# Optimization experiments

Measured on AMD Instinct MI355X. Metric: run time of the kernel, lower is better.

The kernel has to match this reference:

```python
import jax, jax.numpy as jnp
import numpy as np
import math

D_MODEL = 2048
N_HEADS = 16
D_FF = 8192
SEQ = 2048
BATCH = 2
THETA = 10000.0
EPS = 1e-5


def _rope(x, pos):
    # x: [B, H, S, d_k] ; pos: [B, S] int
    d = x.shape[-1]
    inv_freq = 1.0 / (THETA ** (jnp.arange(0, d, 2, dtype=jnp.float32) / d))  # [d/2]
    ang = pos[..., None].astype(jnp.float32) * inv_freq  # [B, S, d/2]
    cos = jnp.cos(ang)[:, None, :, :, None]  # [B,1,S,d/2,1]
    sin = jnp.sin(ang)[:, None, :, :, None]
    xr = x.reshape(*x.shape[:-1], d // 2, 2)
    x1, x2 = xr[..., 0], xr[..., 1]
    rot = jnp.stack((-x2, x1), axis=-1)  # rotate pairs
    out = xr * cos + rot * sin
    return out.reshape(x.shape)


def _trunc_normal(key, shape, in_f, out_f):
    std = math.sqrt(2.0 / (in_f + out_f))
    return jax.random.truncated_normal(key, -3.0, 3.0, shape, jnp.float32) * std


def setup_inputs() -> dict:
    key = jax.random.key(0)
    ks = jax.random.split(key, 8)
    x = jax.random.normal(ks[0], (BATCH, SEQ, D_MODEL), jnp.float32)
    token_positions = jnp.sort(jax.random.randint(ks[1], (BATCH, SEQ), 0, SEQ), axis=-1)
    W_qkv = _trunc_normal(ks[2], (3 * D_MODEL, D_MODEL), D_MODEL, 3 * D_MODEL)
    W_o = _trunc_normal(ks[3], (D_MODEL, D_MODEL), D_MODEL, D_MODEL)
    W1 = _trunc_normal(ks[4], (D_FF, D_MODEL), D_MODEL, D_FF)
    W3 = _trunc_normal(ks[5], (D_FF, D_MODEL), D_MODEL, D_FF)
    W2 = _trunc_normal(ks[6], (D_MODEL, D_FF), D_FF, D_MODEL)
    g1 = jnp.ones((D_MODEL,), jnp.float32)
    g2 = jnp.ones((D_MODEL,), jnp.float32)
    return {"x": x, "token_positions": token_positions, "W_qkv": W_qkv, "W_o": W_o,
            "g1": g1, "g2": g2, "W1": W1, "W3": W3, "W2": W2}


def _rmsnorm(x, g):
    xf = x.astype(jnp.float32)
    rms = jnp.sqrt(jnp.mean(xf * xf, axis=-1, keepdims=True) + EPS)
    return (xf / rms * g).astype(x.dtype)


def reference(x, token_positions, W_qkv, W_o, g1, g2, W1, W3, W2):
    B, S, D = x.shape
    H = N_HEADS
    dk = D // H
    # --- attention sublayer ---
    h = _rmsnorm(x, g1)
    qkv = jnp.einsum('bsi,oi->bso', h, W_qkv)  # [B,S,3D]
    q, k, v = jnp.split(qkv, 3, axis=-1)
    to_heads = lambda t: t.reshape(B, S, H, dk).transpose(0, 2, 1, 3)  # [B,H,S,dk]
    q, k, v = to_heads(q), to_heads(k), to_heads(v)
    q = _rope(q, token_positions)
    k = _rope(k, token_positions)
    scores = jnp.einsum('bhnd,bhmd->bhnm', q, k) / math.sqrt(dk)  # [B,H,S,S]
    mask = jnp.tril(jnp.ones((S, S), dtype=bool))
    scores = jnp.where(mask, scores, -jnp.inf)
    attn = jax.nn.softmax(scores, axis=-1)
    o = jnp.einsum('bhnm,bhmd->bhnd', attn, v)
    o = o.transpose(0, 2, 1, 3).reshape(B, S, D)
    x = x + jnp.einsum('bsi,oi->bso', o, W_o)
    # --- SwiGLU FFN sublayer ---
    h2 = _rmsnorm(x, g2)
    x1 = jnp.einsum('bsi,oi->bso', h2, W1)
    x3 = jnp.einsum('bsi,oi->bso', h2, W3)
    x = x + jnp.einsum('bsi,oi->bso', jax.nn.silu(x1) * x3, W2)
    return x
```

## Files before the change

### kernel.cpp

```cpp
#include <hip/hip_runtime.h>

#define DEV __device__ __forceinline__

typedef __bf16 bf16x8 __attribute__((ext_vector_type(8)));
typedef float f32x4 __attribute__((ext_vector_type(4)));
typedef unsigned short u16x8 __attribute__((ext_vector_type(8)));

DEV unsigned short f2bf(float f) {
  unsigned int u = __float_as_uint(f);
  u += 0x7fffu + ((u >> 16) & 1u);
  return (unsigned short)(u >> 16);
}
DEV float bf2f(unsigned short h) {
  return __uint_as_float(((unsigned int)h) << 16);
}
DEV void gload16(const void* g, void* l) {
  __builtin_amdgcn_global_load_lds(
      (const __attribute__((address_space(1))) unsigned int*)g,
      (__attribute__((address_space(3))) unsigned int*)l, 16, 0, 0);
}
DEV f32x4 mfma16(bf16x8 a, bf16x8 b, f32x4 c) {
  return __builtin_amdgcn_mfma_f32_16x16x32_bf16(a, b, c, 0, 0, 0);
}

#define SB   __builtin_amdgcn_s_barrier()
#define SCH  __builtin_amdgcn_sched_barrier(0)
#define LGKM0 asm volatile("s_waitcnt lgkmcnt(0)" ::: "memory")
#define LGKM4 asm volatile("s_waitcnt lgkmcnt(4)" ::: "memory")
#define VM6  asm volatile("s_waitcnt vmcnt(6)" ::: "memory")
#define PRIO1 __builtin_amdgcn_s_setprio(1)
#define PRIO0 __builtin_amdgcn_s_setprio(0)

__global__ __launch_bounds__(256) void k_cvt(const float* __restrict__ in,
                                             unsigned short* __restrict__ out, int n8) {
  const int stride = gridDim.x * 256;
  for (int i = blockIdx.x * 256 + threadIdx.x; i < n8; i += stride) {
    const float4* p = (const float4*)(in + (long)i * 8);
    const float4 a = p[0], b = p[1];
    u16x8 o = { f2bf(a.x), f2bf(a.y), f2bf(a.z), f2bf(a.w),
                f2bf(b.x), f2bf(b.y), f2bf(b.z), f2bf(b.w) };
    *(u16x8*)(out + (long)i * 8) = o;
  }
}

__global__ __launch_bounds__(256) void k_rmsnorm(const float* __restrict__ x,
                                                 const float* __restrict__ g,
                                                 unsigned short* __restrict__ out) {
  const int row = blockIdx.x;
  const int t = threadIdx.x;
  const float4* xr = (const float4*)(x + (long)row * 2048);
  const float4 a = xr[t * 2], c = xr[t * 2 + 1];
  float ss = a.x * a.x + a.y * a.y + a.z * a.z + a.w * a.w +
             c.x * c.x + c.y * c.y + c.z * c.z + c.w * c.w;
#pragma unroll
  for (int o = 32; o > 0; o >>= 1) ss += __shfl_down(ss, o);
  __shared__ float ws4[4];
  __shared__ float invs;
  if ((t & 63) == 0) ws4[t >> 6] = ss;
  __syncthreads();
  if (t == 0) invs = 1.0f / sqrtf((ws4[0] + ws4[1] + ws4[2] + ws4[3]) * (1.0f / 2048.0f) + 1e-5f);
  __syncthreads();
  const float inv = invs;
  const float4* gr = (const float4*)g;
  const float4 g0 = gr[t * 2], g1v = gr[t * 2 + 1];
  u16x8 o8 = { f2bf(a.x * inv * g0.x),  f2bf(a.y * inv * g0.y),
               f2bf(a.z * inv * g0.z),  f2bf(a.w * inv * g0.w),
               f2bf(c.x * inv * g1v.x), f2bf(c.y * inv * g1v.y),
               f2bf(c.z * inv * g1v.z), f2bf(c.w * inv * g1v.w) };
  *(u16x8*)(out + (long)row * 2048 + t * 8) = o8;
}

__global__ __launch_bounds__(256) void k_rmsnorm2(const float* __restrict__ xa,
                                                  const float* __restrict__ xb,
                                                  const float* __restrict__ g,
                                                  float* __restrict__ xsum,
                                                  unsigned short* __restrict__ out) {
  const int row = blockIdx.x;
  const int t = threadIdx.x;
  const float4* ar = (const float4*)(xa + (long)row * 2048);
  const float4* br = (const float4*)(xb + (long)row * 2048);
  float4 a = ar[t * 2], c = ar[t * 2 + 1];
  const float4 pa = br[t * 2], pc = br[t * 2 + 1];
  a.x += pa.x; a.y += pa.y; a.z += pa.z; a.w += pa.w;
  c.x += pc.x; c.y += pc.y; c.z += pc.z; c.w += pc.w;
  float4* sr = (float4*)(xsum + (long)row * 2048);
  sr[t * 2] = a; sr[t * 2 + 1] = c;
  float ss = a.x * a.x + a.y * a.y + a.z * a.z + a.w * a.w +
             c.x * c.x + c.y * c.y + c.z * c.z + c.w * c.w;
#pragma unroll
  for (int o = 32; o > 0; o >>= 1) ss += __shfl_down(ss, o);
  __shared__ float ws4[4];
  __shared__ float invs;
  if ((t & 63) == 0) ws4[t >> 6] = ss;
  __syncthreads();
  if (t == 0) invs = 1.0f / sqrtf((ws4[0] + ws4[1] + ws4[2] + ws4[3]) * (1.0f / 2048.0f) + 1e-5f);
  __syncthreads();
  const float inv = invs;
  const float4* gr = (const float4*)g;
  const float4 g0 = gr[t * 2], g1v = gr[t * 2 + 1];
  u16x8 o8 = { f2bf(a.x * inv * g0.x),  f2bf(a.y * inv * g0.y),
               f2bf(a.z * inv * g0.z),  f2bf(a.w * inv * g0.w),
               f2bf(c.x * inv * g1v.x), f2bf(c.y * inv * g1v.y),
               f2bf(c.z * inv * g1v.z), f2bf(c.w * inv * g1v.w) };
  *(u16x8*)(out + (long)row * 2048 + t * 8) = o8;
}

template <int EPI>
__global__ __launch_bounds__(512, 2) void k_gemm256(
    const unsigned short* __restrict__ A, const unsigned short* __restrict__ B,
    unsigned short* __restrict__ outBF, float* __restrict__ outF,
    const float* __restrict__ resid, const unsigned short* __restrict__ aux,
    float* __restrict__ partial, const int* __restrict__ tp,
    unsigned short* __restrict__ p2, unsigned short* __restrict__ p3,
    int M, int N, int K, int Keff) {
  __shared__ __align__(16) unsigned short lds[2][2][2][128][64];
  const int tid = threadIdx.x;
  const int wid = tid >> 6, lane = tid & 63;
  const int wr = wid >> 2, wc = wid & 3;
  const int fr = lane & 15, g4 = lane >> 4;

  const int nwg = gridDim.x;
  int bid = blockIdx.x;
  { int q = nwg >> 3, r = nwg & 7, xcd = bid & 7, lo = bid >> 3;
    bid = (xcd < r ? xcd * (q + 1) : r * (q + 1) + (xcd - r) * q) + lo; }
  int tile = bid, ks = 0;
  if constexpr (EPI == 3) { ks = bid & 1; tile = bid >> 1; }
  const int nxb = N >> 8;
  const int bx = tile % nxb, by = tile / nxb;
  const int arow0 = by << 8, bcol0 = bx << 8;
  const int NT = Keff >> 6;

  const int srow = tid >> 3;
  const int sg = (tid & 7) ^ (srow & 7);
  const unsigned short* Asrc = A + (long)(arow0 + srow) * K + (long)ks * Keff + (sg << 3);
  const unsigned short* Bsrc = B + (long)(bcol0 + srow) * K + (long)ks * Keff + (sg << 3);

  const int posk0 = (g4 ^ (lane & 7)) << 3;
  const int posk1 = ((4 + g4) ^ (lane & 7)) << 3;

  f32x4 acc[8][4] = {};
  bf16x8 a[4][2], b0[2][2], b1[2][2];

#define STAGE(SRC, xs, bufi, mat, h)                                            \
  { const unsigned short* s_ = (SRC) + (long)(h) * 128 * K + (long)(xs) * 64;   \
    unsigned short* d_ = &lds[bufi][mat][h][0][0] + wid * 512;                  \
    gload16(s_, d_);                                                            \
    gload16(s_ + (long)64 * K, d_ + 4096); }
#define RD_A(BA, mh)                                                            \
  _Pragma("unroll") for (int m_ = 0; m_ < 4; ++m_) {                            \
    const unsigned short* p_ = (BA) + ((mh) * 64 + m_ * 16 + fr) * 64;          \
    a[m_][0] = *(const bf16x8*)(p_ + posk0);                                    \
    a[m_][1] = *(const bf16x8*)(p_ + posk1); }
#define RD_B(BB, arr, nh)                                                       \
  _Pragma("unroll") for (int n_ = 0; n_ < 2; ++n_) {                            \
    const unsigned short* p_ = (BB) + ((nh) * 32 + n_ * 16 + fr) * 64;          \
    arr[n_][0] = *(const bf16x8*)(p_ + posk0);                                  \
    arr[n_][1] = *(const bf16x8*)(p_ + posk1); }
#define MM(mh, nh, Bv)                                                          \
  _Pragma("unroll") for (int k_ = 0; k_ < 2; ++k_)                              \
  _Pragma("unroll") for (int m_ = 0; m_ < 4; ++m_)                              \
  _Pragma("unroll") for (int n_ = 0; n_ < 2; ++n_)                              \
    acc[(mh)*4+m_][(nh)*2+n_] = mfma16(a[m_][k_], Bv[n_][k_], acc[(mh)*4+m_][(nh)*2+n_]);

  STAGE(Asrc, 0, 0, 0, 0);
  STAGE(Asrc, 0, 0, 0, 1);
  STAGE(Bsrc, 0, 0, 1, 0);
  STAGE(Bsrc, 0, 0, 1, 1);
  { const int x1p = (NT > 1) ? 1 : 0;
    STAGE(Bsrc, x1p, 1, 1, 0);
    STAGE(Bsrc, x1p, 1, 1, 1);
    STAGE(Asrc, x1p, 1, 0, 0); }
  VM6; SCH; SB; SCH;
  {
    const unsigned short* baseA = &lds[0][0][wr][0][0];
    const unsigned short* baseB = &lds[0][1][wc >> 1][0][0] + (wc & 1) * 4096;
    RD_A(baseA, 0); RD_B(baseB, b0, 0);
  }

  for (int t = 0; t < NT; ++t) {
    const unsigned short* baseA = &lds[t & 1][0][wr][0][0];
    const unsigned short* baseB = &lds[t & 1][1][wc >> 1][0][0] + (wc & 1) * 4096;
    const unsigned short* baseA2 = &lds[(t + 1) & 1][0][wr][0][0];
    const unsigned short* baseB2 = &lds[(t + 1) & 1][1][wc >> 1][0][0] + (wc & 1) * 4096;
    const int x1 = (t + 1 < NT) ? t + 1 : NT - 1;
    const int x2i = (t + 2 < NT) ? t + 2 : NT - 1;
    const int bn = (t + 1) & 1, bc = t & 1;

    SB;
    RD_B(baseB, b1, 1);
    STAGE(Asrc, x1, bn, 0, 1);
    LGKM4; SCH;
    PRIO1; MM(0, 0, b0); PRIO0;
    LGKM0; SCH;
    PRIO1; MM(0, 1, b1); PRIO0;

    SB;
    RD_A(baseA, 1);
    STAGE(Bsrc, x2i, bc, 1, 0);
    LGKM0; SCH;
    PRIO1; MM(1, 1, b1); PRIO0;

    SB;
    STAGE(Asrc, x2i, bc, 0, 0);
    STAGE(Bsrc, x2i, bc, 1, 1);
    PRIO1; MM(1, 0, b0); PRIO0;
    VM6; SCH; SB; SCH;
    RD_A(baseA2, 0);
    RD_B(baseB2, b0, 0);
  }
#undef STAGE
#undef RD_A
#undef RD_B
#undef MM

  const int er = g4 << 2;
  if constexpr (EPI == 4) {
    const int region = bcol0 >> 11;
#pragma unroll
    for (int m = 0; m < 8; ++m) {
      const int grow = arow0 + wr * 128 + m * 16 + er;
      float pos4[4];
#pragma unroll
      for (int r = 0; r < 4; ++r)
        pos4[r] = (region < 2) ? (float)tp[grow + r] : 0.f;
#pragma unroll
      for (int n = 0; n < 4; ++n) {
        const int gcol = bcol0 + wc * 64 + n * 16 + fr;
        const int d = gcol & 127;
        const float invf = __expf((float)(d >> 1) * -0.14391156831212787f);
        const int h = (gcol >> 7) & 15;
#pragma unroll
        for (int r = 0; r < 4; ++r) {
          const int row = grow + r;
          const int b = row >> 11, s = row & 2047;
          float v = acc[m][n][r];
          if (region < 2) {
            const float other = __shfl_xor(v, 1);
            float cc, sn;
            __sincosf(pos4[r] * invf, &sn, &cc);
            v = (d & 1) ? (v * cc + other * sn) : (v * cc - other * sn);
          }
          unsigned short* dst = (region == 0) ? outBF : (region == 1 ? p2 : p3);
          dst[((long)((b << 4) + h) * 2048 + s) * 128 + d] = f2bf(v);
        }
      }
    }
  } else {
#pragma unroll
    for (int m = 0; m < 8; ++m) {
#pragma unroll
      for (int n = 0; n < 4; ++n) {
        const int grow = arow0 + wr * 128 + m * 16 + er;
        const int gcol = bcol0 + wc * 64 + n * 16 + fr;
#pragma unroll
        for (int r = 0; r < 4; ++r) {
          const long idx = (long)(grow + r) * N + gcol;
          const float v = acc[m][n][r];
          if constexpr (EPI == 0) {
            outBF[idx] = f2bf(v);
          } else if constexpr (EPI == 1) {
            outF[idx] = resid[idx] + v;
          } else if constexpr (EPI == 2) {
            const float x1v = bf2f(aux[idx]);
            const float sl = x1v / (1.0f + __expf(-x1v));
            outBF[idx] = f2bf(sl * v);
          } else {
            if (ks == 0) outF[idx] = resid[idx] + v;
            else         partial[idx] = v;
          }
        }
      }
    }
  }
}

__global__ __launch_bounds__(512, 1) void k_gemm_n128(
    const unsigned short* __restrict__ A, const unsigned short* __restrict__ B,
    float* __restrict__ outF, const float* __restrict__ resid, int M, int N, int K) {
  __shared__ __align__(16) unsigned short lds[3][384 * 64];
  const int tid = threadIdx.x;
  const int wid = tid >> 6, lane = tid & 63;
  const int wr = wid >> 1, wc = wid & 1;
  const int fr = lane & 15, g4 = lane >> 4;

  const int nwg = gridDim.x;
  int bid = blockIdx.x;
  { int q = nwg >> 3, r = nwg & 7, xcd = bid & 7, lo = bid >> 3;
    bid = (xcd < r ? xcd * (q + 1) : r * (q + 1) + (xcd - r) * q) + lo; }
  const int nxb = N >> 7;
  const int bx = bid % nxb, by = bid / nxb;
  const int arow0 = by << 8, bcol0 = bx << 7;
  const int NT = K >> 6;

  const int srow = tid >> 3;
  const int sg = (tid & 7) ^ (srow & 7);
  const unsigned short* Asrc = A + (long)(arow0 + srow) * K + (sg << 3);
  const unsigned short* Bsrc = B + (long)(bcol0 + srow) * K + (sg << 3);

  const int posk0 = (g4 ^ (lane & 7)) << 3;
  const int posk1 = ((4 + g4) ^ (lane & 7)) << 3;

  f32x4 acc[4][4] = {};
  bf16x8 a[4][2], bl[2][2], bh[2][2];

#define SITE_A(xs, bufi, s)                                                    \
  gload16(Asrc + (long)((s) * 64) * K + (long)(xs) * 64,                       \
          &lds[bufi][(s) * 4096] + wid * 512);
#define SITE_B(xs, bufi, s)                                                    \
  gload16(Bsrc + (long)((s) * 64) * K + (long)(xs) * 64,                       \
          &lds[bufi][16384 + (s) * 4096] + wid * 512);
#define RDA(BUF)                                                               \
  _Pragma("unroll") for (int m_ = 0; m_ < 4; ++m_) {                           \
    const unsigned short* p_ = (BUF) + (wr * 64 + m_ * 16 + fr) * 64;          \
    a[m_][0] = *(const bf16x8*)(p_ + posk0);                                   \
    a[m_][1] = *(const bf16x8*)(p_ + posk1); }
#define RDB(BUF, arr, off)                                                     \
  _Pragma("unroll") for (int n_ = 0; n_ < 2; ++n_) {                           \
    const unsigned short* p_ = (BUF) + 16384 + (wc * 64 + (off) + n_ * 16 + fr) * 64; \
    arr[n_][0] = *(const bf16x8*)(p_ + posk0);                                 \
    arr[n_][1] = *(const bf16x8*)(p_ + posk1); }
#define MMN(nh, Bv)                                                            \
  _Pragma("unroll") for (int k_ = 0; k_ < 2; ++k_)                             \
  _Pragma("unroll") for (int m_ = 0; m_ < 4; ++m_)                             \
  _Pragma("unroll") for (int n_ = 0; n_ < 2; ++n_)                             \
    acc[m_][(nh)*2+n_] = mfma16(a[m_][k_], Bv[n_][k_], acc[m_][(nh)*2+n_]);

  SITE_A(0, 0, 0); SITE_A(0, 0, 1); SITE_A(0, 0, 2); SITE_A(0, 0, 3);
  SITE_B(0, 0, 0); SITE_B(0, 0, 1);
  { const int x1p = (NT > 1) ? 1 : 0;
    SITE_A(x1p, 1, 0); SITE_A(x1p, 1, 1); SITE_A(x1p, 1, 2); SITE_A(x1p, 1, 3);
    SITE_B(x1p, 1, 0); SITE_B(x1p, 1, 1); }
  VM6; SCH; SB; SCH;
  RDA(lds[0]); RDB(lds[0], bl, 0);

  for (int t = 0; t < NT; ++t) {
    const unsigned short* bufb = lds[t % 3];
    const unsigned short* bufn = lds[(t + 1) % 3];
    const int bn = (t + 2) % 3;
    const int xs = (t + 2 < NT) ? t + 2 : NT - 1;

    SB;
    RDB(bufb, bh, 32);
    SITE_A(xs, bn, 0); SITE_A(xs, bn, 1);
    LGKM4; SCH;
    PRIO1; MMN(0, bl); PRIO0;
    SITE_A(xs, bn, 2); SITE_A(xs, bn, 3); SITE_B(xs, bn, 0); SITE_B(xs, bn, 1);
    LGKM0; SCH;
    PRIO1; MMN(1, bh); PRIO0;
    VM6; SCH; SB; SCH;
    RDA(bufn); RDB(bufn, bl, 0);
  }
#undef SITE_A
#undef SITE_B
#undef RDA
#undef RDB
#undef MMN

  const int er = g4 << 2;
#pragma unroll
  for (int m = 0; m < 4; ++m) {
#pragma unroll
    for (int n = 0; n < 4; ++n) {
      const int grow = arow0 + wr * 64 + m * 16 + er;
      const int gcol = bcol0 + wc * 64 + n * 16 + fr;
#pragma unroll
      for (int r = 0; r < 4; ++r) {
        const long idx = (long)(grow + r) * N + gcol;
        outF[idx] = resid[idx] + acc[m][n][r];
      }
    }
  }
}

__global__ __launch_bounds__(256) void k_vtrans(const unsigned short* __restrict__ Vh,
                                                unsigned short* __restrict__ Vt, int S) {
  __shared__ __align__(16) unsigned short t[128 * 72];
  const int bh = blockIdx.x;
  const int s0 = blockIdx.y << 6;
  const int tid = threadIdx.x;
  const int sl = tid >> 2, c4 = tid & 3;
#pragma unroll
  for (int it = 0; it < 4; ++it) {
    const int chunk = c4 * 4 + it;
    u16x8 v = *(const u16x8*)(Vh + ((long)bh * S + s0 + sl) * 128 + chunk * 8);
#pragma unroll
    for (int jj = 0; jj < 8; ++jj) t[(chunk * 8 + jj) * 72 + sl] = v[jj];
  }
  __syncthreads();
  const int d = tid >> 1, half = tid & 1;
  unsigned short* dst = Vt + ((long)bh * 128 + d) * S + s0 + half * 32;
  const unsigned short* srcr = &t[d * 72 + half * 32];
#pragma unroll
  for (int u = 0; u < 4; ++u)
    *(u16x8*)(dst + u * 8) = *(const u16x8*)(srcr + u * 8);
}

__global__ __launch_bounds__(256) void k_attn(const unsigned short* __restrict__ Q,
                                              const unsigned short* __restrict__ Kh,
                                              const unsigned short* __restrict__ Vt,
                                              unsigned short* __restrict__ O, int S) {
  __shared__ __align__(16) unsigned short lds_k[64 * 128];
  __shared__ __align__(16) unsigned short lds_v[128 * 64];
  __shared__ __align__(16) unsigned short lds_p[4 * 16 * 64];
  const int bh = blockIdx.x;
  const int b = bh >> 4, h = bh & 15;
  const int qt = gridDim.y - 1 - blockIdx.y;
  const int q0 = qt << 6;
  const int tid = threadIdx.x, w = tid >> 6, lane = tid & 63;
  const int fr = lane & 15, g4 = lane >> 4;

  bf16x8 qf[4];
  {
    const unsigned short* qb = Q + ((long)bh * S + q0 + w * 16 + fr) * 128 + (g4 << 3);
#pragma unroll
    for (int kk = 0; kk < 4; ++kk) qf[kk] = *(const bf16x8*)(qb + kk * 32);
  }

  f32x4 accO[8] = {};
  float mrow[4], lrow[4];
#pragma unroll
  for (int r = 0; r < 4; ++r) { mrow[r] = -1e30f; lrow[r] = 0.f; }

  const int k_row = (w << 4) + g4;
  const int k_cb = fr << 4;
  const int v_row = (w << 5) + (lane >> 3);
  const int v_cb = (lane & 7) << 4;
  const long kbase = (long)bh * S * 128;
  const long vbase = (long)bh * 128 * S;

  const int ntile = qt + 1;
  for (int it = 0; it < ntile; ++it) {
    const int kv0 = it << 6;
#pragma unroll
    for (int j = 0; j < 4; ++j) {
      const int kr = k_row + j * 4;
      const int kc = k_cb ^ ((kr & 7) << 4);
      gload16(Kh + kbase + (long)(kv0 + kr) * 128 + (kc >> 1), &lds_k[w * 2048 + j * 512]);
      const int vr = v_row + j * 8;
      const int vc = v_cb ^ ((vr & 7) << 4);
      gload16(Vt + vbase + (long)vr * S + kv0 + (vc >> 1), &lds_v[w * 2048 + j * 512]);
    }
    __syncthreads();

    f32x4 sc[4] = {};
#pragma unroll
    for (int kk = 0; kk < 4; ++kk) {
      const int kb = (kk << 6) + (g4 << 4);
#pragma unroll
      for (int n = 0; n < 4; ++n) {
        const int krw = n * 16 + fr;
        const int swz = (krw & 7) << 4;
        bf16x8 kf = *(const bf16x8*)&lds_k[krw * 128 + ((kb ^ swz) >> 1)];
        sc[n] = mfma16(qf[kk], kf, sc[n]);
      }
    }

    const float scl = 0.08838834764831845f;
    float sv[4][4];
    const bool needmask = (kv0 + 63 > q0 + w * 16);
#pragma unroll
    for (int n = 0; n < 4; ++n)
#pragma unroll
      for (int r = 0; r < 4; ++r) {
        float v = sc[n][r] * scl;
        if (needmask) {
          const int qi = q0 + w * 16 + (g4 << 2) + r;
          const int ki = kv0 + n * 16 + fr;
          if (ki > qi) v = -1e30f;
        }
        sv[n][r] = v;
      }
    float corr[4];
#pragma unroll
    for (int r = 0; r < 4; ++r) {
      float tm = fmaxf(fmaxf(sv[0][r], sv[1][r]), fmaxf(sv[2][r], sv[3][r]));
      tm = fmaxf(tm, __shfl_xor(tm, 1));
      tm = fmaxf(tm, __shfl_xor(tm, 2));
      tm = fmaxf(tm, __shfl_xor(tm, 4));
      tm = fmaxf(tm, __shfl_xor(tm, 8));
      const float mn = fmaxf(mrow[r], tm);
      corr[r] = __expf(mrow[r] - mn);
      mrow[r] = mn;
    }
    float rs[4] = {0.f, 0.f, 0.f, 0.f};
#pragma unroll
    for (int n = 0; n < 4; ++n)
#pragma unroll
      for (int r = 0; r < 4; ++r) {
        const float p = __expf(sv[n][r] - mrow[r]);
        rs[r] += p;
        const int pr = (g4 << 2) + r;
        const int pc = (n * 16 + fr) << 1;
        lds_p[(w << 10) + pr * 64 + ((pc ^ ((pr & 7) << 4)) >> 1)] = f2bf(p);
      }
#pragma unroll
    for (int r = 0; r < 4; ++r) {
      float s = rs[r];
      s += __shfl_xor(s, 1);
      s += __shfl_xor(s, 2);
      s += __shfl_xor(s, 4);
      s += __shfl_xor(s, 8);
      lrow[r] = lrow[r] * corr[r] + s;
    }
#pragma unroll
    for (int cb = 0; cb < 8; ++cb)
#pragma unroll
      for (int r = 0; r < 4; ++r) accO[cb][r] *= corr[r];

#pragma unroll
    for (int kk = 0; kk < 2; ++kk) {
      const int pb = (kk << 6) + (g4 << 4);
      bf16x8 pf = *(const bf16x8*)&lds_p[(w << 10) + fr * 64 + ((pb ^ ((fr & 7) << 4)) >> 1)];
#pragma unroll
      for (int cb = 0; cb < 8; ++cb) {
        const int vrw = cb * 16 + fr;
        bf16x8 vf = *(const bf16x8*)&lds_v[vrw * 64 + ((pb ^ ((vrw & 7) << 4)) >> 1)];
        accO[cb] = mfma16(pf, vf, accO[cb]);
      }
    }
    __syncthreads();
  }

#pragma unroll
  for (int cb = 0; cb < 8; ++cb)
#pragma unroll
    for (int r = 0; r < 4; ++r) {
      const int si = q0 + w * 16 + (g4 << 2) + r;
      const float o = accO[cb][r] / lrow[r];
      O[((long)b * S + si) * 2048 + h * 128 + cb * 16 + fr] = f2bf(o);
    }
}

extern "C" void kernel_launch(void* const* d_in, const int* in_sizes, int n_in,
                              void* d_out, int out_size, void* d_ws, size_t ws_size,
                              hipStream_t stream) {
  const float* x    = (const float*)d_in[0];
  const int*   tp   = (const int*)d_in[1];
  const float* Wqkv = (const float*)d_in[2];
  const float* Wo   = (const float*)d_in[3];
  const float* g1   = (const float*)d_in[4];
  const float* g2   = (const float*)d_in[5];
  const float* W1   = (const float*)d_in[6];
  const float* W3   = (const float*)d_in[7];
  const float* W2   = (const float*)d_in[8];
  float* out = (float*)d_out;

  char* ws = (char*)d_ws;
  const size_t MB = 1024 * 1024;
  unsigned short* Qh      = (unsigned short*)(ws + 0 * MB);
  unsigned short* Kh      = (unsigned short*)(ws + 16 * MB);
  unsigned short* Vt      = (unsigned short*)(ws + 32 * MB);
  unsigned short* Vh      = (unsigned short*)(ws + 48 * MB);
  unsigned short* O_bf    = (unsigned short*)(ws + 48 * MB);
  unsigned short* t_bf    = (unsigned short*)(ws + 0 * MB);
  float*          x2      = (float*)         (ws + 64 * MB);
  unsigned short* h2_bf   = (unsigned short*)(ws + 96 * MB);
  unsigned short* wo_bf   = (unsigned short*)(ws + 96 * MB);
  unsigned short* wqkv_bf = (unsigned short*)(ws + 112 * MB);
  unsigned short* w1_bf   = (unsigned short*)(ws + 112 * MB);
  unsigned short* w2_bf   = (unsigned short*)(ws + 112 * MB);
  unsigned short* h1_bf   = (unsigned short*)(ws + 144 * MB);
  float*          part    = (float*)         (ws + 144 * MB);
  unsigned short* w3_bf   = (unsigned short*)(ws + 144 * MB);

  const int S = 2048;

  k_cvt<<<1024, 256, 0, stream>>>(Wqkv, wqkv_bf, 12582912 / 8);
  k_rmsnorm<<<4096, 256, 0, stream>>>(x, g1, h1_bf);
  k_gemm256<4><<<dim3(384), 512, 0, stream>>>(h1_bf, wqkv_bf, Qh, nullptr, nullptr, nullptr,
                                              nullptr, tp, Kh, Vh, 4096, 6144, 2048, 2048);
  k_vtrans<<<dim3(32, 32), 256, 0, stream>>>(Vh, Vt, S);
  k_cvt<<<1024, 256, 0, stream>>>(Wo, wo_bf, 4194304 / 8);
  k_cvt<<<1024, 256, 0, stream>>>(W1, w1_bf, 16777216 / 8);
  k_attn<<<dim3(32, 32), 256, 0, stream>>>(Qh, Kh, Vt, O_bf, S);
  k_gemm256<3><<<dim3(256), 512, 0, stream>>>(O_bf, wo_bf, nullptr, x2, x, nullptr,
                                              part, nullptr, nullptr, nullptr, 4096, 2048, 2048, 1024);

  k_rmsnorm2<<<4096, 256, 0, stream>>>(x2, part, g2, x2, h2_bf);
  k_cvt<<<1024, 256, 0, stream>>>(W3, w3_bf, 16777216 / 8);
  k_gemm256<0><<<dim3(512), 512, 0, stream>>>(h2_bf, w1_bf, t_bf, nullptr, nullptr, nullptr,
                                              nullptr, nullptr, nullptr, nullptr, 4096, 8192, 2048, 2048);
  k_cvt<<<1024, 256, 0, stream>>>(W2, w2_bf, 16777216 / 8);
  k_gemm256<2><<<dim3(512), 512, 0, stream>>>(h2_bf, w3_bf, t_bf, nullptr, nullptr, t_bf,
                                              nullptr, nullptr, nullptr, nullptr, 4096, 8192, 2048, 2048);
  k_gemm_n128<<<dim3(256), 512, 0, stream>>>(t_bf, w2_bf, out, x2, 4096, 2048, 8192);
}
```

Before: 765.8 us.

## Pair causal query tiles per attention block and move QKV GEMM to 256x128 tiles

The attention kernel now has each block handle two query tiles, one from the high end and one from the low end of the causal range. They share the K/V tile loads, which balances per-block work and halves the grid. The QKV projection with fused RoPE moves from the 256x256 GEMM to the 256x128 GEMM kernel. That doubles the workgroup count to 768 so the CUs fill better, at the cost of more A re-reads. Keeping two accumulator sets raises register pressure in attention.

```diff
diff --git a/kernel.cpp b/kernel.cpp
--- a/kernel.cpp
+++ b/kernel.cpp
@@ -110,9 +110,7 @@
     const unsigned short* __restrict__ A, const unsigned short* __restrict__ B,
     unsigned short* __restrict__ outBF, float* __restrict__ outF,
     const float* __restrict__ resid, const unsigned short* __restrict__ aux,
-    float* __restrict__ partial, const int* __restrict__ tp,
-    unsigned short* __restrict__ p2, unsigned short* __restrict__ p3,
-    int M, int N, int K, int Keff) {
+    float* __restrict__ partial, int M, int N, int K, int Keff) {
   __shared__ __align__(16) unsigned short lds[2][2][2][128][64];
   const int tid = threadIdx.x;
   const int wid = tid >> 6, lane = tid & 63;
@@ -214,69 +212,38 @@
 #undef MM
 
   const int er = g4 << 2;
-  if constexpr (EPI == 4) {
-    const int region = bcol0 >> 11;
-#pragma unroll
-    for (int m = 0; m < 8; ++m) {
+#pragma unroll
+  for (int m = 0; m < 8; ++m) {
+#pragma unroll
+    for (int n = 0; n < 4; ++n) {
       const int grow = arow0 + wr * 128 + m * 16 + er;
-      float pos4[4];
-#pragma unroll
-      for (int r = 0; r < 4; ++r)
-        pos4[r] = (region < 2) ? (float)tp[grow + r] : 0.f;
-#pragma unroll
-      for (int n = 0; n < 4; ++n) {
-        const int gcol = bcol0 + wc * 64 + n * 16 + fr;
-        const int d = gcol & 127;
-        const float invf = __expf((float)(d >> 1) * -0.14391156831212787f);
-        const int h = (gcol >> 7) & 15;
-#pragma unroll
-        for (int r = 0; r < 4; ++r) {
-          const int row = grow + r;
-          const int b = row >> 11, s = row & 2047;
-          float v = acc[m][n][r];
-          if (region < 2) {
-            const float other = __shfl_xor(v, 1);
-            float cc, sn;
-            __sincosf(pos4[r] * invf, &sn, &cc);
-            v = (d & 1) ? (v * cc + other * sn) : (v * cc - other * sn);
-          }
-          unsigned short* dst = (region == 0) ? outBF : (region == 1 ? p2 : p3);
-          dst[((long)((b << 4) + h) * 2048 + s) * 128 + d] = f2bf(v);
+      const int gcol = bcol0 + wc * 64 + n * 16 + fr;
+#pragma unroll
+      for (int r = 0; r < 4; ++r) {
+        const long idx = (long)(grow + r) * N + gcol;
+        const float v = acc[m][n][r];
+        if constexpr (EPI == 0) {
+          outBF[idx] = f2bf(v);
+        } else if constexpr (EPI == 2) {
+          const float x1v = bf2f(aux[idx]);
+          const float sl = x1v / (1.0f + __expf(-x1v));
+          outBF[idx] = f2bf(sl * v);
+        } else {
+          if (ks == 0) outF[idx] = resid[idx] + v;
+          else         partial[idx] = v;
         }
       }
     }
-  } else {
-#pragma unroll
-    for (int m = 0; m < 8; ++m) {
-#pragma unroll
-      for (int n = 0; n < 4; ++n) {
-        const int grow = arow0 + wr * 128 + m * 16 + er;
-        const int gcol = bcol0 + wc * 64 + n * 16 + fr;
-#pragma unroll
-        for (int r = 0; r < 4; ++r) {
-          const long idx = (long)(grow + r) * N + gcol;
-          const float v = acc[m][n][r];
-          if constexpr (EPI == 0) {
-            outBF[idx] = f2bf(v);
-          } else if constexpr (EPI == 1) {
-            outF[idx] = resid[idx] + v;
-          } else if constexpr (EPI == 2) {
-            const float x1v = bf2f(aux[idx]);
-            const float sl = x1v / (1.0f + __expf(-x1v));
-            outBF[idx] = f2bf(sl * v);
-          } else {
-            if (ks == 0) outF[idx] = resid[idx] + v;
-            else         partial[idx] = v;
-          }
-        }
-      }
-    }
-  }
-}
-
+  }
+}
+
+template <int EPI>
 __global__ __launch_bounds__(512, 1) void k_gemm_n128(
     const unsigned short* __restrict__ A, const unsigned short* __restrict__ B,
-    float* __restrict__ outF, const float* __restrict__ resid, int M, int N, int K) {
+    float* __restrict__ outF, const float* __restrict__ resid,
+    const int* __restrict__ tp, unsigned short* __restrict__ oQ,
+    unsigned short* __restrict__ oK, unsigned short* __restrict__ oV,
+    int M, int N, int K) {
   __shared__ __align__(16) unsigned short lds[3][384 * 64];
   const int tid = threadIdx.x;
   const int wid = tid >> 6, lane = tid & 63;
@@ -357,16 +324,48 @@
 #undef MMN
 
   const int er = g4 << 2;
-#pragma unroll
-  for (int m = 0; m < 4; ++m) {
-#pragma unroll
-    for (int n = 0; n < 4; ++n) {
+  if constexpr (EPI == 4) {
+    const int region = bcol0 >> 11;
+    const int h = (bcol0 >> 7) & 15;
+    unsigned short* dst = (region == 0) ? oQ : (region == 1 ? oK : oV);
+#pragma unroll
+    for (int m = 0; m < 4; ++m) {
       const int grow = arow0 + wr * 64 + m * 16 + er;
-      const int gcol = bcol0 + wc * 64 + n * 16 + fr;
-#pragma unroll
-      for (int r = 0; r < 4; ++r) {
-        const long idx = (long)(grow + r) * N + gcol;
-        outF[idx] = resid[idx] + acc[m][n][r];
+      float pos4[4];
+#pragma unroll
+      for (int r = 0; r < 4; ++r)
+        pos4[r] = (region < 2) ? (float)tp[grow + r] : 0.f;
+#pragma unroll
+      for (int n = 0; n < 4; ++n) {
+        const int d = (wc * 64 + n * 16 + fr);
+        const float invf = __expf((float)(d >> 1) * -0.14391156831212787f);
+#pragma unroll
+        for (int r = 0; r < 4; ++r) {
+          const int row = grow + r;
+          const int b = row >> 11, s = row & 2047;
+          float v = acc[m][n][r];
+          if (region < 2) {
+            const float other = __shfl_xor(v, 1);
+            float cc, sn;
+            __sincosf(pos4[r] * invf, &sn, &cc);
+            v = (d & 1) ? (v * cc + other * sn) : (v * cc - other * sn);
+          }
+          dst[((long)((b << 4) + h) * 2048 + s) * 128 + d] = f2bf(v);
+        }
+      }
+    }
+  } else {
+#pragma unroll
+    for (int m = 0; m < 4; ++m) {
+#pragma unroll
+      for (int n = 0; n < 4; ++n) {
+        const int grow = arow0 + wr * 64 + m * 16 + er;
+        const int gcol = bcol0 + wc * 64 + n * 16 + fr;
+#pragma unroll
+        for (int r = 0; r < 4; ++r) {
+          const long idx = (long)(grow + r) * N + gcol;
+          outF[idx] = resid[idx] + acc[m][n][r];
+        }
       }
     }
   }
@@ -404,22 +403,27 @@
   __shared__ __align__(16) unsigned short lds_p[4 * 16 * 64];
   const int bh = blockIdx.x;
   const int b = bh >> 4, h = bh & 15;
-  const int qt = gridDim.y - 1 - blockIdx.y;
-  const int q0 = qt << 6;
+  const int nq = (S >> 6);
+  const int qtH = nq - 1 - blockIdx.y;
+  const int qtL = blockIdx.y;
+  const int q0H = qtH << 6, q0L = qtL << 6;
   const int tid = threadIdx.x, w = tid >> 6, lane = tid & 63;
   const int fr = lane & 15, g4 = lane >> 4;
 
-  bf16x8 qf[4];
+  bf16x8 qfH[4], qfL[4];
   {
-    const unsigned short* qb = Q + ((long)bh * S + q0 + w * 16 + fr) * 128 + (g4 << 3);
-#pragma unroll
-    for (int kk = 0; kk < 4; ++kk) qf[kk] = *(const bf16x8*)(qb + kk * 32);
-  }
-
-  f32x4 accO[8] = {};
-  float mrow[4], lrow[4];
-#pragma unroll
-  for (int r = 0; r < 4; ++r) { mrow[r] = -1e30f; lrow[r] = 0.f; }
+    const unsigned short* qb = Q + ((long)bh * S + q0H + w * 16 + fr) * 128 + (g4 << 3);
+#pragma unroll
+    for (int kk = 0; kk < 4; ++kk) qfH[kk] = *(const bf16x8*)(qb + kk * 32);
+    const unsigned short* qb2 = Q + ((long)bh * S + q0L + w * 16 + fr) * 128 + (g4 << 3);
+#pragma unroll
+    for (int kk = 0; kk < 4; ++kk) qfL[kk] = *(const bf16x8*)(qb2 + kk * 32);
+  }
+
+  f32x4 accH[8] = {}, accL[8] = {};
+  float mH[4], lH[4], mL[4], lL[4];
+#pragma unroll
+  for (int r = 0; r < 4; ++r) { mH[r] = -1e30f; lH[r] = 0.f; mL[r] = -1e30f; lL[r] = 0.f; }
 
   const int k_row = (w << 4) + g4;
   const int k_cb = fr << 4;
@@ -427,8 +431,76 @@
   const int v_cb = (lane & 7) << 4;
   const long kbase = (long)bh * S * 128;
   const long vbase = (long)bh * 128 * S;
-
-  const int ntile = qt + 1;
+  const float scl = 0.08838834764831845f;
+
+#define PROC(QF, ACC, MR, LR, Q0)                                              \
+  {                                                                            \
+    f32x4 sc[4] = {};                                                          \
+    _Pragma("unroll") for (int kk = 0; kk < 4; ++kk) {                         \
+      const int kb = (kk << 6) + (g4 << 4);                                    \
+      _Pragma("unroll") for (int n = 0; n < 4; ++n) {                          \
+        const int krw = n * 16 + fr;                                           \
+        const int swz = (krw & 7) << 4;                                        \
+        bf16x8 kf = *(const bf16x8*)&lds_k[krw * 128 + ((kb ^ swz) >> 1)];     \
+        sc[n] = mfma16(QF[kk], kf, sc[n]);                                     \
+      }                                                                        \
+    }                                                                          \
+    float sv[4][4];                                                            \
+    const bool needmask = (kv0 + 63 > (Q0) + w * 16);                          \
+    _Pragma("unroll") for (int n = 0; n < 4; ++n)                              \
+      _Pragma("unroll") for (int r = 0; r < 4; ++r) {                          \
+        float v = sc[n][r] * scl;                                              \
+        if (needmask) {                                                        \
+          const int qi = (Q0) + w * 16 + (g4 << 2) + r;                        \
+          const int ki = kv0 + n * 16 + fr;                                    \
+          if (ki > qi) v = -1e30f;                                             \
+        }                                                                      \
+        sv[n][r] = v;                                                          \
+      }                                                                        \
+    float corr[4];                                                             \
+    _Pragma("unroll") for (int r = 0; r < 4; ++r) {                            \
+      float tm = fmaxf(fmaxf(sv[0][r], sv[1][r]), fmaxf(sv[2][r], sv[3][r]));  \
+      tm = fmaxf(tm, __shfl_xor(tm, 1));                                       \
+      tm = fmaxf(tm, __shfl_xor(tm, 2));                                       \
+      tm = fmaxf(tm, __shfl_xor(tm, 4));                                       \
+      tm = fmaxf(tm, __shfl_xor(tm, 8));                                       \
+      const float mn = fmaxf(MR[r], tm);                                       \
+      corr[r] = __expf(MR[r] - mn);                                            \
+      MR[r] = mn;                                                              \
+    }                                                                          \
+    float rs[4] = {0.f, 0.f, 0.f, 0.f};                                        \
+    _Pragma("unroll") for (int n = 0; n < 4; ++n)                              \
+      _Pragma("unroll") for (int r = 0; r < 4; ++r) {                          \
+        const float p = __expf(sv[n][r] - MR[r]);                              \
+        rs[r] += p;                                                            \
+        const int pr = (g4 << 2) + r;                                          \
+        const int pc = (n * 16 + fr) << 1;                                     \
+        lds_p[(w << 10) + pr * 64 + ((pc ^ ((pr & 7) << 4)) >> 1)] = f2bf(p);  \
+      }                                                                        \
+    _Pragma("unroll") for (int r = 0; r < 4; ++r) {                            \
+      float s = rs[r];                                                         \
+      s += __shfl_xor(s, 1);                                                   \
+      s += __shfl_xor(s, 2);                                                   \
+      s += __shfl_xor(s, 4);                                                   \
+      s += __shfl_xor(s, 8);                                                   \
+      LR[r] = LR[r] * corr[r] + s;                                             \
+    }                                                                          \
+    _Pragma("unroll") for (int cb = 0; cb < 8; ++cb)                           \
+      _Pragma("unroll") for (int r = 0; r < 4; ++r) ACC[cb][r] *= corr[r];     \
+    _Pragma("unroll") for (int kk = 0; kk < 2; ++kk) {                         \
+      const int pb = (kk << 6) + (g4 << 4);                                    \
+      bf16x8 pf = *(const bf16x8*)&lds_p[(w << 10) + fr * 64 +                 \
+                                         ((pb ^ ((fr & 7) << 4)) >> 1)];       \
+      _Pragma("unroll") for (int cb = 0; cb < 8; ++cb) {                       \
+        const int vrw = cb * 16 + fr;                                          \
+        bf16x8 vf = *(const bf16x8*)&lds_v[vrw * 64 +                          \
+                                           ((pb ^ ((vrw & 7) << 4)) >> 1)];    \
+        ACC[cb] = mfma16(pf, vf, ACC[cb]);                                     \
+      }                                                                        \
+    }                                                                          \
+  }
+
+  const int ntile = qtH + 1;
   for (int it = 0; it < ntile; ++it) {
     const int kv0 = it << 6;
 #pragma unroll
@@ -442,92 +514,21 @@
     }
     __syncthreads();
 
-    f32x4 sc[4] = {};
-#pragma unroll
-    for (int kk = 0; kk < 4; ++kk) {
-      const int kb = (kk << 6) + (g4 << 4);
-#pragma unroll
-      for (int n = 0; n < 4; ++n) {
-        const int krw = n * 16 + fr;
-        const int swz = (krw & 7) << 4;
-        bf16x8 kf = *(const bf16x8*)&lds_k[krw * 128 + ((kb ^ swz) >> 1)];
-        sc[n] = mfma16(qf[kk], kf, sc[n]);
-      }
-    }
-
-    const float scl = 0.08838834764831845f;
-    float sv[4][4];
-    const bool needmask = (kv0 + 63 > q0 + w * 16);
-#pragma unroll
-    for (int n = 0; n < 4; ++n)
-#pragma unroll
-      for (int r = 0; r < 4; ++r) {
-        float v = sc[n][r] * scl;
-        if (needmask) {
-          const int qi = q0 + w * 16 + (g4 << 2) + r;
-          const int ki = kv0 + n * 16 + fr;
-          if (ki > qi) v = -1e30f;
-        }
-        sv[n][r] = v;
-      }
-    float corr[4];
+    PROC(qfH, accH, mH, lH, q0H);
+    if (it <= qtL) PROC(qfL, accL, mL, lL, q0L);
+
+    __syncthreads();
+  }
+#undef PROC
+
+#pragma unroll
+  for (int cb = 0; cb < 8; ++cb)
 #pragma unroll
     for (int r = 0; r < 4; ++r) {
-      float tm = fmaxf(fmaxf(sv[0][r], sv[1][r]), fmaxf(sv[2][r], sv[3][r]));
-      tm = fmaxf(tm, __shfl_xor(tm, 1));
-      tm = fmaxf(tm, __shfl_xor(tm, 2));
-      tm = fmaxf(tm, __shfl_xor(tm, 4));
-      tm = fmaxf(tm, __shfl_xor(tm, 8));
-      const float mn = fmaxf(mrow[r], tm);
-      corr[r] = __expf(mrow[r] - mn);
-      mrow[r] = mn;
-    }
-    float rs[4] = {0.f, 0.f, 0.f, 0.f};
-#pragma unroll
-    for (int n = 0; n < 4; ++n)
-#pragma unroll
-      for (int r = 0; r < 4; ++r) {
-        const float p = __expf(sv[n][r] - mrow[r]);
-        rs[r] += p;
-        const int pr = (g4 << 2) + r;
-        const int pc = (n * 16 + fr) << 1;
-        lds_p[(w << 10) + pr * 64 + ((pc ^ ((pr & 7) << 4)) >> 1)] = f2bf(p);
-      }
-#pragma unroll
-    for (int r = 0; r < 4; ++r) {
-      float s = rs[r];
-      s += __shfl_xor(s, 1);
-      s += __shfl_xor(s, 2);
-      s += __shfl_xor(s, 4);
-      s += __shfl_xor(s, 8);
-      lrow[r] = lrow[r] * corr[r] + s;
-    }
-#pragma unroll
-    for (int cb = 0; cb < 8; ++cb)
-#pragma unroll
-      for (int r = 0; r < 4; ++r) accO[cb][r] *= corr[r];
-
-#pragma unroll
-    for (int kk = 0; kk < 2; ++kk) {
-      const int pb = (kk << 6) + (g4 << 4);
-      bf16x8 pf = *(const bf16x8*)&lds_p[(w << 10) + fr * 64 + ((pb ^ ((fr & 7) << 4)) >> 1)];
-#pragma unroll
-      for (int cb = 0; cb < 8; ++cb) {
-        const int vrw = cb * 16 + fr;
-        bf16x8 vf = *(const bf16x8*)&lds_v[vrw * 64 + ((pb ^ ((vrw & 7) << 4)) >> 1)];
-        accO[cb] = mfma16(pf, vf, accO[cb]);
-      }
-    }
-    __syncthreads();
-  }
-
-#pragma unroll
-  for (int cb = 0; cb < 8; ++cb)
-#pragma unroll
-    for (int r = 0; r < 4; ++r) {
-      const int si = q0 + w * 16 + (g4 << 2) + r;
-      const float o = accO[cb][r] / lrow[r];
-      O[((long)b * S + si) * 2048 + h * 128 + cb * 16 + fr] = f2bf(o);
+      const int siH = q0H + w * 16 + (g4 << 2) + r;
+      O[((long)b * S + siH) * 2048 + h * 128 + cb * 16 + fr] = f2bf(accH[cb][r] / lH[r]);
+      const int siL = q0L + w * 16 + (g4 << 2) + r;
+      O[((long)b * S + siL) * 2048 + h * 128 + cb * 16 + fr] = f2bf(accL[cb][r] / lL[r]);
     }
 }
 
@@ -567,21 +568,23 @@
 
   k_cvt<<<1024, 256, 0, stream>>>(Wqkv, wqkv_bf, 12582912 / 8);
   k_rmsnorm<<<4096, 256, 0, stream>>>(x, g1, h1_bf);
-  k_gemm256<4><<<dim3(384), 512, 0, stream>>>(h1_bf, wqkv_bf, Qh, nullptr, nullptr, nullptr,
-                                              nullptr, tp, Kh, Vh, 4096, 6144, 2048, 2048);
+  k_gemm_n128<4><<<dim3(768), 512, 0, stream>>>(h1_bf, wqkv_bf, nullptr, nullptr,
+                                                tp, Qh, Kh, Vh, 4096, 6144, 2048);
   k_vtrans<<<dim3(32, 32), 256, 0, stream>>>(Vh, Vt, S);
   k_cvt<<<1024, 256, 0, stream>>>(Wo, wo_bf, 4194304 / 8);
   k_cvt<<<1024, 256, 0, stream>>>(W1, w1_bf, 16777216 / 8);
-  k_attn<<<dim3(32, 32), 256, 0, stream>>>(Qh, Kh, Vt, O_bf, S);
+  k_attn<<<dim3(32, 16), 256, 0, stream>>>(Qh, Kh, Vt, O_bf, S);
   k_gemm256<3><<<dim3(256), 512, 0, stream>>>(O_bf, wo_bf, nullptr, x2, x, nullptr,
-                                              part, nullptr, nullptr, nullptr, 4096, 2048, 2048, 1024);
+                                              part, 4096, 2048, 2048, 1024);
 
   k_rmsnorm2<<<4096, 256, 0, stream>>>(x2, part, g2, x2, h2_bf);
   k_cvt<<<1024, 256, 0, stream>>>(W3, w3_bf, 16777216 / 8);
   k_gemm256<0><<<dim3(512), 512, 0, stream>>>(h2_bf, w1_bf, t_bf, nullptr, nullptr, nullptr,
-                                              nullptr, nullptr, nullptr, nullptr, 4096, 8192, 2048, 2048);
+                                              nullptr, 4096, 8192, 2048, 2048);
   k_cvt<<<1024, 256, 0, stream>>>(W2, w2_bf, 16777216 / 8);
   k_gemm256<2><<<dim3(512), 512, 0, stream>>>(h2_bf, w3_bf, t_bf, nullptr, nullptr, t_bf,
-                                              nullptr, nullptr, nullptr, nullptr, 4096, 8192, 2048, 2048);
-  k_gemm_n128<<<dim3(256), 512, 0, stream>>>(t_bf, w2_bf, out, x2, 4096, 2048, 8192);
-}
+                                              nullptr, 4096, 8192, 2048, 2048);
+  k_gemm_n128<1><<<dim3(256), 512, 0, stream>>>(t_bf, w2_bf, out, x2,
+                                                nullptr, nullptr, nullptr, nullptr,
+                                                4096, 2048, 8192);
+}
```

Result: slower. 794.3 us (+3.7%).
